# Performance work log

Measured on AMD Instinct MI355X. Metric: run time of the kernel, lower is better.

Reference implementation:

```python
import jax, jax.numpy as jnp
import numpy as np

HEAD_SIZE = 128


def setup_inputs() -> dict:
    key = jax.random.key(0)
    k0, k1, k2, k3 = jax.random.split(key, 4)
    B, S, E, H = 4, 4096, 1024, HEAD_SIZE
    x = jax.random.normal(k0, (B, S, E), dtype=jnp.float32)
    scale = 1.0 / np.sqrt(E).astype(np.float32)
    Wq = jax.random.normal(k1, (E, H), dtype=jnp.float32) * scale
    Wk = jax.random.normal(k2, (E, H), dtype=jnp.float32) * scale
    Wv = jax.random.normal(k3, (E, H), dtype=jnp.float32) * scale
    k_mask = jnp.ones((B, S), dtype=jnp.int32)
    return {"x": x, "Wq": Wq, "Wk": Wk, "Wv": Wv, "k_mask": k_mask}


def reference(x, Wq, Wk, Wv, k_mask):
    # Self-attention path (kv=None), causal=True
    Q = x @ Wq  # [B, S, H]
    K = x @ Wk  # [B, S, H]
    V = x @ Wv  # [B, S, H]
    inv_sqrt_h = np.float32(1.0 / np.sqrt(HEAD_SIZE))
    att = jnp.einsum('bqh,bkh->bqk', Q, K) * inv_sqrt_h  # [B, S, S]
    neg_inf = jnp.float32(-jnp.inf)
    # padding mask over keys: [B, 1, S_k]
    att = jnp.where(k_mask[:, None, :] == 0, neg_inf, att)
    # causal mask: tril over (q_len, k_len)
    S = Q.shape[1]
    c_mask = jnp.tril(jnp.ones((S, S), dtype=bool))  # [S, S]
    att = jnp.where(c_mask[None, :, :], att, neg_inf)
    att = jax.nn.softmax(att, axis=-1)
    return att @ V  # [B, S, H]
```

## Files before the change

kernel.cpp:

```cpp
#include <hip/hip_runtime.h>
#include <hip/hip_bf16.h>

typedef unsigned short u16;
typedef __attribute__((ext_vector_type(8))) short bf16x8;
typedef __attribute__((ext_vector_type(4))) float f32x4;
typedef __attribute__((ext_vector_type(4))) unsigned short u16x4;

#define SQ 4096
#define HQ 128
#define NCHUNK 144

__device__ __forceinline__ u16 f2b(float f) {
  unsigned int u = __float_as_uint(f);
  unsigned int r = (u + 0x7fffu + ((u >> 16) & 1u)) >> 16;
  return (u16)r;
}

__device__ __forceinline__ u16 f2b_fast(float f) {
  __hip_bfloat16 h = __float2bfloat16(f);
  return __builtin_bit_cast(u16, h);
}

__device__ __forceinline__ float b2f(u16 v) {
  unsigned int u = ((unsigned int)v) << 16;
  return __uint_as_float(u);
}

__device__ __forceinline__ void gload_lds16(const u16* gsrc, u16* ldst) {
  __builtin_amdgcn_global_load_lds((const __attribute__((address_space(1))) void*)gsrc,
                                   (__attribute__((address_space(3))) void*)ldst, 16, 0, 0);
}

__global__ __launch_bounds__(256) void k_wt(const float* __restrict__ Wq, const float* __restrict__ Wk,
                                            const float* __restrict__ Wv, u16* __restrict__ wt) {
  int idx = blockIdx.x * 256 + threadIdx.x;
  int z = idx >> 17, r = idx & 131071, n = r >> 10, k = r & 1023;
  const float* W = (z == 0) ? Wq : (z == 1) ? Wk : Wv;
  wt[idx] = f2b(W[k * 128 + n]);
}

__global__ __launch_bounds__(256, 3) void k_proj(const float* __restrict__ x, const u16* __restrict__ wt,
                                                 u16* __restrict__ qb, u16* __restrict__ kb,
                                                 u16* __restrict__ vt) {
  int blk = blockIdx.x;
  int t = threadIdx.x;
  int wn = t >> 6, lane = t & 63;
  int lr = lane & 15, lg = lane >> 4;

  __shared__ __align__(16) u16 xl[2][32 * 32];
  __shared__ __align__(16) u16 wl[2][384 * 32];

  int srow = t >> 3, sc8 = t & 7;
  const float* xg = x + (long)(blk * 32 + srow) * 1024 + sc8 * 4;
  int xch = ((sc8 >> 1) ^ ((srow >> 1) & 3));
  int xoff = srow * 32 + xch * 8 + (sc8 & 1) * 4;

  f32x4 acc[2][6];
#pragma unroll
  for (int i = 0; i < 2; ++i)
#pragma unroll
    for (int j = 0; j < 6; ++j) acc[i][j] = (f32x4){0.f, 0.f, 0.f, 0.f};

  auto stage_w = [&](int bufi, int k0) {
#pragma unroll
    for (int i = 0; i < 6; ++i) {
      int ci = i * 256 + t;
      int row = ci >> 2, ch = ci & 3;
      gload_lds16(wt + (long)row * 1024 + k0 + ((ch ^ ((row >> 1) & 3)) << 3),
                  &wl[bufi][0] + ci * 8);
    }
  };

  {
    float4 xa = *(const float4*)(xg);
    stage_w(0, 0);
    u16x4 o;
    o[0] = f2b(xa.x); o[1] = f2b(xa.y); o[2] = f2b(xa.z); o[3] = f2b(xa.w);
    *(u16x4*)(&xl[0][0] + xoff) = o;
  }
  __syncthreads();

  for (int ks = 0; ks < 32; ++ks) {
    int cur = ks & 1;
    float4 xa;
    bool more = (ks + 1 < 32);
    if (more) {
      xa = *(const float4*)(xg + (ks + 1) * 32);
      stage_w(cur ^ 1, (ks + 1) * 32);
    }
    bf16x8 af[2], bf[6];
#pragma unroll
    for (int i = 0; i < 2; ++i) {
      int row = i * 16 + lr;
      af[i] = *(const bf16x8*)(&xl[cur][0] + row * 32 + ((lg ^ ((row >> 1) & 3)) << 3));
    }
#pragma unroll
    for (int j = 0; j < 6; ++j) {
      int row = wn * 96 + j * 16 + lr;
      bf[j] = *(const bf16x8*)(&wl[cur][0] + row * 32 + ((lg ^ ((row >> 1) & 3)) << 3));
    }
#pragma unroll
    for (int i = 0; i < 2; ++i)
#pragma unroll
      for (int j = 0; j < 6; ++j)
        acc[i][j] = __builtin_amdgcn_mfma_f32_16x16x32_bf16(af[i], bf[j], acc[i][j], 0, 0, 0);
    if (more) {
      u16x4 o;
      o[0] = f2b(xa.x); o[1] = f2b(xa.y); o[2] = f2b(xa.z); o[3] = f2b(xa.w);
      *(u16x4*)(&xl[cur ^ 1][0] + xoff) = o;
    }
    __syncthreads();
  }

#pragma unroll
  for (int i = 0; i < 2; ++i)
#pragma unroll
    for (int j = 0; j < 6; ++j)
#pragma unroll
      for (int r = 0; r < 4; ++r) {
        int m = blk * 32 + i * 16 + lg * 4 + r;
        int col = wn * 96 + j * 16 + lr;
        int z = col >> 7, cz = col & 127;
        u16 v = f2b(acc[i][j][r]);
        if (z == 0) qb[(long)m * 128 + cz] = v;
        else if (z == 1) kb[(long)m * 128 + cz] = v;
        else { int bb = m >> 12, sR = m & 4095; vt[(long)bb * 524288 + (long)cz * 4096 + sR] = v; }
      }
}

__global__ __launch_bounds__(512, 4) void k_attn(const u16* __restrict__ qb, const u16* __restrict__ kb,
                                                 const u16* __restrict__ vt, const int* __restrict__ kmask,
                                                 u16* __restrict__ po, float* __restrict__ pl) {
  const float SCALE_LOG2 = 0.08838834764831845f * 1.4426950408889634f;
  const float MFIX = 24.0f;
  int f = (NCHUNK - 1) - (int)blockIdx.x;
  int b = blockIdx.y;
  int qt2 = 0, cum = 0;
  while (cum + ((qt2 + 4) >> 2) <= f) { cum += (qt2 + 4) >> 2; ++qt2; }
  int kc = f - cum;
  int ntile = 2 * qt2 + 2;
  int kt0 = kc * 8;
  int kt1 = min(kt0 + 8, ntile);

  int t = threadIdx.x, w = t >> 6, lane = t & 63;
  int lr = lane & 15, lg = lane >> 4, sw = lr & 7;
  int qrow0 = qt2 * 128 + w * 16;
  const u16* Q = qb + ((long)(b * SQ + qrow0)) * HQ;
  const u16* K = kb + (long)b * SQ * HQ;
  const u16* V = vt + (long)b * HQ * SQ;
  const int* msk = kmask + b * SQ;

  __shared__ __align__(16) u16 Kl[2][64 * 128];
  __shared__ __align__(16) u16 Vl[2][128 * 64];
  __shared__ __align__(16) u16 plds[8][16 * 64];

  bf16x8 aq[4];
#pragma unroll
  for (int c = 0; c < 4; ++c) aq[c] = *(const bf16x8*)(Q + lr * HQ + c * 32 + lg * 8);

  bf16x8 ones;
#pragma unroll
  for (int e = 0; e < 8; ++e) ones[e] = (short)0x3F80;

  f32x4 o[8];
#pragma unroll
  for (int n = 0; n < 8; ++n) o[n] = (f32x4){0.f, 0.f, 0.f, 0.f};
  f32x4 l_acc = (f32x4){0.f, 0.f, 0.f, 0.f};

  auto stage = [&](int bufi, int kb0) {
    const u16* Kg = K + (long)kb0 * HQ;
    const u16* Vg = V + kb0;
#pragma unroll
    for (int i = 0; i < 2; ++i) {
      int ci = w * 2 + i;
      int o16 = ci * 64 + lane;
      int row = o16 >> 4, ch = o16 & 15;
      gload_lds16(Kg + row * HQ + ((ch ^ (row & 7)) << 3), &Kl[bufi][ci * 512]);
    }
#pragma unroll
    for (int i = 0; i < 2; ++i) {
      int ci = w * 2 + i;
      int o16 = ci * 64 + lane;
      int row = o16 >> 3, ch = o16 & 7;
      gload_lds16(Vg + (long)row * SQ + ((ch ^ (row & 7)) << 3), &Vl[bufi][ci * 512]);
    }
  };

  stage(0, kt0 * 64);
  __syncthreads();

  u16* pw = &plds[w][0];
  for (int kt = kt0; kt < kt1; ++kt) {
    int cur = (kt - kt0) & 1;
    int kb0 = kt * 64;
    if (kt + 1 < kt1) stage(cur ^ 1, kb0 + 64);

    if (kb0 <= qrow0 + 15) {
      f32x4 s[4];
#pragma unroll
      for (int h = 0; h < 4; ++h) {
        f32x4 acc = (f32x4){0.f, 0.f, 0.f, 0.f};
        const u16* Kp = &Kl[cur][(h * 16 + lr) * 128];
#pragma unroll
        for (int c = 0; c < 4; ++c) {
          bf16x8 bk = *(const bf16x8*)(Kp + (((c * 4 + lg) ^ sw) << 3));
          acc = __builtin_amdgcn_mfma_f32_16x16x32_bf16(aq[c], bk, acc, 0, 0, 0);
        }
        s[h] = acc;
      }
      float mf[4];
#pragma unroll
      for (int h = 0; h < 4; ++h) mf[h] = (msk[kb0 + h * 16 + lr] != 0) ? 1.0f : 0.0f;
      bool needc = (kb0 + 63 > qrow0);
#pragma unroll
      for (int r = 0; r < 4; ++r) {
        int row = lg * 4 + r;
        int qr = qrow0 + row;
#pragma unroll
        for (int h = 0; h < 4; ++h) {
          float p = __builtin_exp2f(fmaf(s[h][r], SCALE_LOG2, -MFIX)) * mf[h];
          if (needc) p = ((kb0 + h * 16 + lr) <= qr) ? p : 0.0f;
          int poff = row * 64 + ((((h * 2 + (lr >> 3)) ^ (row & 7))) << 3) + (lr & 7);
          pw[poff] = f2b_fast(p);
        }
      }
      bf16x8 ap0 = *(const bf16x8*)(pw + lr * 64 + ((lg ^ sw) << 3));
      bf16x8 ap1 = *(const bf16x8*)(pw + lr * 64 + (((4 + lg) ^ sw) << 3));
      l_acc = __builtin_amdgcn_mfma_f32_16x16x32_bf16(ap0, ones, l_acc, 0, 0, 0);
      l_acc = __builtin_amdgcn_mfma_f32_16x16x32_bf16(ap1, ones, l_acc, 0, 0, 0);
#pragma unroll
      for (int n = 0; n < 8; ++n) {
        const u16* Vp = &Vl[cur][(n * 16 + lr) * 64];
        bf16x8 bv0 = *(const bf16x8*)(Vp + ((lg ^ sw) << 3));
        bf16x8 bv1 = *(const bf16x8*)(Vp + (((4 + lg) ^ sw) << 3));
        o[n] = __builtin_amdgcn_mfma_f32_16x16x32_bf16(ap0, bv0, o[n], 0, 0, 0);
        o[n] = __builtin_amdgcn_mfma_f32_16x16x32_bf16(ap1, bv1, o[n], 0, 0, 0);
      }
    }
    __syncthreads();
  }

  long p = (long)b * NCHUNK + f;
  u16* pob = po + p * 16384;
#pragma unroll
  for (int n = 0; n < 8; ++n)
#pragma unroll
    for (int r = 0; r < 4; ++r)
      pob[(w * 16 + lg * 4 + r) * 128 + n * 16 + lr] = f2b_fast(o[n][r]);
  if (lr == 0) {
#pragma unroll
    for (int r = 0; r < 4; ++r) pl[p * 128 + w * 16 + lg * 4 + r] = l_acc[r];
  }
}

__global__ __launch_bounds__(256) void k_merge(const u16* __restrict__ po, const float* __restrict__ pl,
                                               float* __restrict__ out) {
  int qt2 = blockIdx.x, b = blockIdx.y;
  int nch = (qt2 + 4) >> 2;
  int pre = 0;
  for (int q = 0; q < qt2; ++q) pre += (q + 4) >> 2;
  long pbase = (long)b * NCHUNK + pre;
  int t = threadIdx.x;
  int row = t >> 1, c0 = (t & 1) * 64;
  float l = 0.f;
  for (int i = 0; i < nch; ++i) l += pl[(pbase + i) * 128 + row];
  float inv = 1.0f / l;
  const u16* p0 = po + pbase * 16384 + row * 128 + c0;
  float* orow = out + ((long)(b * SQ + qt2 * 128 + row)) * HQ + c0;
#pragma unroll
  for (int j = 0; j < 64; j += 4) {
    float acc0 = 0.f, acc1 = 0.f, acc2 = 0.f, acc3 = 0.f;
    for (int i = 0; i < nch; ++i) {
      u16x4 v = *(const u16x4*)(p0 + (long)i * 16384 + j);
      acc0 += b2f(v[0]); acc1 += b2f(v[1]); acc2 += b2f(v[2]); acc3 += b2f(v[3]);
    }
    float4 r = {acc0 * inv, acc1 * inv, acc2 * inv, acc3 * inv};
    *(float4*)(orow + j) = r;
  }
}

extern "C" void kernel_launch(void* const* d_in, const int* in_sizes, int n_in,
                              void* d_out, int out_size, void* d_ws, size_t ws_size,
                              hipStream_t stream) {
  const float* x  = (const float*)d_in[0];
  const float* Wq = (const float*)d_in[1];
  const float* Wk = (const float*)d_in[2];
  const float* Wv = (const float*)d_in[3];
  const int* kmask = (const int*)d_in[4];
  char* ws = (char*)d_ws;
  u16* wt = (u16*)(ws + 33554432);
  u16* qb = (u16*)(ws + 34340864);
  u16* kb = (u16*)(ws + 38535168);
  u16* vt = (u16*)(ws + 42729472);
  u16* po = (u16*)ws;
  float* pl = (float*)(ws + 33554432);
  float* out = (float*)d_out;

  k_wt<<<1536, 256, 0, stream>>>(Wq, Wk, Wv, wt);
  k_proj<<<512, 256, 0, stream>>>(x, wt, qb, kb, vt);
  k_attn<<<dim3(NCHUNK, 4), 512, 0, stream>>>(qb, kb, vt, kmask, po, pl);
  k_merge<<<dim3(32, 4), 256, 0, stream>>>(po, pl, out);
}
```

Before: 136.1 us.

## Retile projection GEMM to 64x192 tiles with deeper x prefetch

The projection kernel is restructured from 32-row by 384-column tiles on 4 waves into 64-row by 192-column tiles on 8 waves (2x4 wave grid), launched over a 2D grid that splits the output columns in half. The fp32 x loads are prefetched two k-steps ahead in registers, and x is converted to bf16 with the intrinsic instead of manual rounding. The aim is more parallelism and better hiding of global load latency. The cost is that x is now read twice (once per column half). The partial-sum buffer pointer is also moved to a new workspace offset, which could overlap other buffers. A leftover helper lambda is defined but never used.

```diff
diff --git a/kernel.cpp b/kernel.cpp
--- a/kernel.cpp
+++ b/kernel.cpp
@@ -39,87 +39,99 @@
   wt[idx] = f2b(W[k * 128 + n]);
 }
 
-__global__ __launch_bounds__(256, 3) void k_proj(const float* __restrict__ x, const u16* __restrict__ wt,
+__global__ __launch_bounds__(512, 4) void k_proj(const float* __restrict__ x, const u16* __restrict__ wt,
                                                  u16* __restrict__ qb, u16* __restrict__ kb,
                                                  u16* __restrict__ vt) {
-  int blk = blockIdx.x;
+  int mt = blockIdx.x, nh = blockIdx.y;
   int t = threadIdx.x;
-  int wn = t >> 6, lane = t & 63;
+  int w = t >> 6, lane = t & 63;
+  int wm = w >> 2, wn = w & 3;
   int lr = lane & 15, lg = lane >> 4;
 
-  __shared__ __align__(16) u16 xl[2][32 * 32];
-  __shared__ __align__(16) u16 wl[2][384 * 32];
+  __shared__ __align__(16) u16 xl[2][64 * 32];
+  __shared__ __align__(16) u16 wl[2][192 * 32];
 
   int srow = t >> 3, sc8 = t & 7;
-  const float* xg = x + (long)(blk * 32 + srow) * 1024 + sc8 * 4;
+  const float* xg = x + (long)(mt * 64 + srow) * 1024 + sc8 * 4;
   int xch = ((sc8 >> 1) ^ ((srow >> 1) & 3));
   int xoff = srow * 32 + xch * 8 + (sc8 & 1) * 4;
 
-  f32x4 acc[2][6];
+  f32x4 acc[2][3];
 #pragma unroll
   for (int i = 0; i < 2; ++i)
 #pragma unroll
-    for (int j = 0; j < 6; ++j) acc[i][j] = (f32x4){0.f, 0.f, 0.f, 0.f};
+    for (int j = 0; j < 3; ++j) acc[i][j] = (f32x4){0.f, 0.f, 0.f, 0.f};
+
+  const u16* wbase = wt + (long)(nh * 192) * 1024;
 
   auto stage_w = [&](int bufi, int k0) {
 #pragma unroll
-    for (int i = 0; i < 6; ++i) {
-      int ci = i * 256 + t;
-      int row = ci >> 2, ch = ci & 3;
-      gload_lds16(wt + (long)row * 1024 + k0 + ((ch ^ ((row >> 1) & 3)) << 3),
-                  &wl[bufi][0] + ci * 8);
+    for (int i = 0; i < 2; ++i) {
+      int ci = i * 512 + t;
+      if (ci < 768) {
+        int row = ci >> 2, ch = ci & 3;
+        gload_lds16(wbase + (long)row * 1024 + k0 + ((ch ^ ((row >> 1) & 3)) << 3),
+                    &wl[bufi][0] + ci * 8);
+      }
     }
   };
 
+  auto xwrite = [&](int bufi, float4 a, float4 b2) {
+    u16x4 o0, o1;
+    o0[0] = f2b_fast(a.x); o0[1] = f2b_fast(a.y); o0[2] = f2b_fast(a.z); o0[3] = f2b_fast(a.w);
+    o1[0] = f2b_fast(b2.x); o1[1] = f2b_fast(b2.y); o1[2] = f2b_fast(b2.z); o1[3] = f2b_fast(b2.w);
+    *(u16x4*)(&xl[bufi][0] + xoff) = (sc8 & 1) ? o0 : o0;
+  };
+
   {
-    float4 xa = *(const float4*)(xg);
+    float4 a0 = *(const float4*)(xg);
     stage_w(0, 0);
     u16x4 o;
-    o[0] = f2b(xa.x); o[1] = f2b(xa.y); o[2] = f2b(xa.z); o[3] = f2b(xa.w);
+    o[0] = f2b_fast(a0.x); o[1] = f2b_fast(a0.y); o[2] = f2b_fast(a0.z); o[3] = f2b_fast(a0.w);
     *(u16x4*)(&xl[0][0] + xoff) = o;
   }
+  float4 p0 = *(const float4*)(xg + 32);
+  float4 p1 = *(const float4*)(xg + 64);
   __syncthreads();
 
   for (int ks = 0; ks < 32; ++ks) {
     int cur = ks & 1;
-    float4 xa;
-    bool more = (ks + 1 < 32);
-    if (more) {
-      xa = *(const float4*)(xg + (ks + 1) * 32);
+    float4 p2;
+    if (ks + 3 < 32) p2 = *(const float4*)(xg + (ks + 3) * 32);
+    if (ks + 1 < 32) {
       stage_w(cur ^ 1, (ks + 1) * 32);
-    }
-    bf16x8 af[2], bf[6];
+      u16x4 o;
+      o[0] = f2b_fast(p0.x); o[1] = f2b_fast(p0.y); o[2] = f2b_fast(p0.z); o[3] = f2b_fast(p0.w);
+      *(u16x4*)(&xl[cur ^ 1][0] + xoff) = o;
+    }
+    bf16x8 af[2], bfr[3];
 #pragma unroll
     for (int i = 0; i < 2; ++i) {
-      int row = i * 16 + lr;
+      int row = wm * 32 + i * 16 + lr;
       af[i] = *(const bf16x8*)(&xl[cur][0] + row * 32 + ((lg ^ ((row >> 1) & 3)) << 3));
     }
 #pragma unroll
-    for (int j = 0; j < 6; ++j) {
-      int row = wn * 96 + j * 16 + lr;
-      bf[j] = *(const bf16x8*)(&wl[cur][0] + row * 32 + ((lg ^ ((row >> 1) & 3)) << 3));
+    for (int j = 0; j < 3; ++j) {
+      int row = wn * 48 + j * 16 + lr;
+      bfr[j] = *(const bf16x8*)(&wl[cur][0] + row * 32 + ((lg ^ ((row >> 1) & 3)) << 3));
     }
 #pragma unroll
     for (int i = 0; i < 2; ++i)
 #pragma unroll
-      for (int j = 0; j < 6; ++j)
-        acc[i][j] = __builtin_amdgcn_mfma_f32_16x16x32_bf16(af[i], bf[j], acc[i][j], 0, 0, 0);
-    if (more) {
-      u16x4 o;
-      o[0] = f2b(xa.x); o[1] = f2b(xa.y); o[2] = f2b(xa.z); o[3] = f2b(xa.w);
-      *(u16x4*)(&xl[cur ^ 1][0] + xoff) = o;
-    }
+      for (int j = 0; j < 3; ++j)
+        acc[i][j] = __builtin_amdgcn_mfma_f32_16x16x32_bf16(af[i], bfr[j], acc[i][j], 0, 0, 0);
+    p0 = p1; p1 = p2;
     __syncthreads();
   }
 
 #pragma unroll
   for (int i = 0; i < 2; ++i)
 #pragma unroll
-    for (int j = 0; j < 6; ++j)
+    for (int j = 0; j < 3; ++j)
 #pragma unroll
       for (int r = 0; r < 4; ++r) {
-        int m = blk * 32 + i * 16 + lg * 4 + r;
-        int col = wn * 96 + j * 16 + lr;
+        int m = mt * 64 + wm * 32 + i * 16 + lg * 4 + r;
+        int col = nh * 192 + wn * 48 + j * 16 + lr;
         int z = col >> 7, cz = col & 127;
         u16 v = f2b(acc[i][j][r]);
         if (z == 0) qb[(long)m * 128 + cz] = v;
@@ -293,11 +305,11 @@
   u16* kb = (u16*)(ws + 38535168);
   u16* vt = (u16*)(ws + 42729472);
   u16* po = (u16*)ws;
-  float* pl = (float*)(ws + 33554432);
+  float* pl = (float*)(ws + 31195136);
   float* out = (float*)d_out;
 
   k_wt<<<1536, 256, 0, stream>>>(Wq, Wk, Wv, wt);
-  k_proj<<<512, 256, 0, stream>>>(x, wt, qb, kb, vt);
+  k_proj<<<dim3(256, 2), 512, 0, stream>>>(x, wt, qb, kb, vt);
   k_attn<<<dim3(NCHUNK, 4), 512, 0, stream>>>(qb, kb, vt, kmask, po, pl);
   k_merge<<<dim3(32, 4), 256, 0, stream>>>(po, pl, out);
 }
```

Measured after the change: 117.4 us. -13.7%, faster.
